# Kernel tuning notes

Hardware: AMD Instinct MI355X
Metric: run time of the kernel (lower is better)

Reference implementation:

```python
import jax, jax.numpy as jnp
import numpy as np

D_IN = 784
D_Z = 100
N_SAMP = 10
LOG_2PI = float(np.log(2.0 * np.pi))


def setup_inputs() -> dict:
    key = jax.random.key(0)
    ks = jax.random.split(key, 8)
    B = 16384
    x = jax.random.uniform(ks[0], (B, D_IN), dtype=jnp.float32)
    s = 0.05  # small init scale so softplus/sigmoid stay in a sane range
    W0 = jax.random.normal(ks[1], (D_Z, D_IN), dtype=jnp.float32) * s
    b0 = jax.random.normal(ks[2], (D_Z,), dtype=jnp.float32) * s
    W1 = jax.random.normal(ks[3], (D_Z, D_IN), dtype=jnp.float32) * s
    b1 = jax.random.normal(ks[4], (D_Z,), dtype=jnp.float32) * s
    W2 = jax.random.normal(ks[5], (D_IN, D_Z), dtype=jnp.float32) * s
    b2 = jax.random.normal(ks[6], (D_IN,), dtype=jnp.float32) * s
    eps = jax.random.normal(ks[7], (N_SAMP, D_Z), dtype=jnp.float32)  # pz.sample([10])
    return {"x": x, "W0": W0, "b0": b0, "W1": W1, "b1": b1, "W2": W2, "b2": b2, "eps": eps}


def reference(x, W0, b0, W1, b1, W2, b2, eps):
    # encoder: per-dim mean over the batch of softplus(Linear(x))
    mean = jnp.mean(jax.nn.softplus(x @ W0.T + b0), axis=0)        # [D_Z]
    cov = jnp.mean(jax.nn.softplus(x @ W1.T + b1), axis=0)         # [D_Z] (diag variances)
    # z = mean + covariance * eps, eps ~ N(0, I)
    z = mean + cov * eps                                           # [N_SAMP, D_Z]
    y = z @ W2.T + b2                                              # [N_SAMP, D_IN]
    p = jax.nn.sigmoid((2.0 * x[:, None, :] - 1.0) * y[None, :, :])  # [B, N_SAMP, D_IN]
    pv_z = jnp.prod(p, axis=-1) + 0.001                            # [B, N_SAMP]
    E_px_v = jnp.mean(jnp.log(pv_z))
    # diagonal-Gaussian log probs (equivalent to the MVN with eye*cov)
    log_pz = -0.5 * jnp.sum(z * z, axis=-1) - 0.5 * D_Z * LOG_2PI
    log_q = (-0.5 * jnp.sum((z - mean) ** 2 / cov, axis=-1)
             - 0.5 * jnp.sum(jnp.log(cov)) - 0.5 * D_Z * LOG_2PI)
    Dkl = jnp.mean(log_pz - log_q)
    return -(E_px_v + Dkl)
```

## Files before the change

kernel.cpp:

```cpp
#include <hip/hip_runtime.h>
#include <hip/hip_bf16.h>
#include <math.h>

#define NROWS 16384
#define DIN   784
#define DZ    100
#define NS    10
#define NCT   16
#define KTILES 25
#define BND_THR 45.0f

typedef unsigned short ushort_t;
typedef short bf16x8 __attribute__((ext_vector_type(8)));
typedef float f32x4  __attribute__((ext_vector_type(4)));

#define WS_Y2 208
#define WS_Z  8064
#define WB_OFF_BYTES (64u * 1024u)

__device__ __forceinline__ float softplus_fast(float v) {
    float t = v * 1.44269504088896f;
    return (fmaxf(t, 0.f)
            + __builtin_amdgcn_logf(1.f + __builtin_amdgcn_exp2f(-fabsf(t))))
           * 0.69314718055995f;
}
__device__ __forceinline__ unsigned pack2(float lo, float hi) {
    float2 f2; f2.x = lo; f2.y = hi;
    __hip_bfloat162 h2 = __float22bfloat162_rn(f2);
    return *reinterpret_cast<unsigned*>(&h2);
}

__global__ __launch_bounds__(256) void wb_kernel(
    const float* __restrict__ W0, const float* __restrict__ W1, ushort_t* __restrict__ Wb)
{
    int t = blockIdx.x * 256 + threadIdx.x;
    if (t >= KTILES * NCT * 64) return;
    int kt = t >> 10;
    int r  = t & 1023;
    int ct = r >> 6, l = r & 63;
    int col = ct * 16 + (l & 15);
    int k0  = kt * 32 + (l >> 4) * 8;
    uint4 o = make_uint4(0u, 0u, 0u, 0u);
    if (col < 200 && k0 < DIN) {
        const float* src = (col < 100 ? W0 + (size_t)col * DIN
                                      : W1 + (size_t)(col - 100) * DIN) + k0;
        float4 a = *(const float4*)src;
        float4 b = *(const float4*)(src + 4);
        o.x = pack2(a.x, a.y); o.y = pack2(a.z, a.w);
        o.z = pack2(b.x, b.y); o.w = pack2(b.z, b.w);
    }
    *(uint4*)(Wb + (size_t)t * 8) = o;
}

__global__ __launch_bounds__(512) void colmean_f(
    const float* __restrict__ x, const ushort_t* __restrict__ Wb,
    const float* __restrict__ b0, const float* __restrict__ b1,
    float* __restrict__ ws)
{
    __shared__ ushort_t xls[2 * KTILES * 512];
    const int tid = threadIdx.x;
    const int lane = tid & 63, w = tid >> 6;
    const int row0 = blockIdx.x * 32;

    for (int slot = tid; slot < 3200; slot += 512) {
        int r  = slot / 100;
        int sl = slot - r * 100;
        int kt = sl >> 2, kc = sl & 3;
        int k0 = kt * 32 + kc * 8;
        uint4 o = make_uint4(0u, 0u, 0u, 0u);
        if (k0 + 8 <= DIN) {
            const float* src = x + (size_t)(row0 + r) * DIN + k0;
            float4 a = *(const float4*)src, b = *(const float4*)(src + 4);
            o.x = pack2(a.x, a.y); o.y = pack2(a.z, a.w);
            o.z = pack2(b.x, b.y); o.w = pack2(b.z, b.w);
        }
        int l = (kc << 4) | (r & 15);
        *(uint4*)&xls[((size_t)(r >> 4) * KTILES + kt) * 512 + l * 8] = o;
    }
    __syncthreads();

    const int ct0 = w * 2;
    const ushort_t* a0p = xls + lane * 8;
    const ushort_t* a1p = xls + KTILES * 512 + lane * 8;
    const ushort_t* wbp = Wb + (size_t)ct0 * 512 + lane * 8;

    f32x4 acc00 = (f32x4){0.f,0.f,0.f,0.f}, acc01 = acc00;
    f32x4 acc10 = acc00, acc11 = acc00;

    bf16x8 A0a, A1a, A0b, A1b;
    uint4  B0a, B1a, B0b, B1b;

    auto ld = [&](int kt, bf16x8& A0, bf16x8& A1, uint4& B0, uint4& B1) {
        A0 = *(const bf16x8*)(a0p + (size_t)kt * 512);
        A1 = *(const bf16x8*)(a1p + (size_t)kt * 512);
        B0 = *(const uint4*)(wbp + (size_t)kt * 8192);
        B1 = *(const uint4*)(wbp + (size_t)kt * 8192 + 512);
    };
    auto cp = [&](const bf16x8& A0, const bf16x8& A1, const uint4& B0, const uint4& B1) {
        bf16x8 f0 = *(const bf16x8*)&B0, f1 = *(const bf16x8*)&B1;
        acc00 = __builtin_amdgcn_mfma_f32_16x16x32_bf16(A0, f0, acc00, 0, 0, 0);
        acc01 = __builtin_amdgcn_mfma_f32_16x16x32_bf16(A0, f1, acc01, 0, 0, 0);
        acc10 = __builtin_amdgcn_mfma_f32_16x16x32_bf16(A1, f0, acc10, 0, 0, 0);
        acc11 = __builtin_amdgcn_mfma_f32_16x16x32_bf16(A1, f1, acc11, 0, 0, 0);
    };

    ld(0, A0a, A1a, B0a, B1a);
    for (int i = 0; i < 12; ++i) {
        ld(2 * i + 1, A0b, A1b, B0b, B1b);
        cp(A0a, A1a, B0a, B1a);
        ld(2 * i + 2, A0a, A1a, B0a, B1a);
        cp(A0b, A1b, B0b, B1b);
    }
    cp(A0a, A1a, B0a, B1a);

    const int jcol = lane & 15;
#pragma unroll
    for (int ctl = 0; ctl < 2; ++ctl) {
        int j = (ct0 + ctl) * 16 + jcol;
        float bias = (j < 100) ? b0[j] : ((j < 200) ? b1[j - 100] : 0.f);
        f32x4 u0 = ctl ? acc01 : acc00;
        f32x4 u1 = ctl ? acc11 : acc10;
        float v = 0.f;
#pragma unroll
        for (int r = 0; r < 4; ++r)
            v += softplus_fast(u0[r] + bias) + softplus_fast(u1[r] + bias);
        v += __shfl_xor(v, 16);
        v += __shfl_xor(v, 32);
        if ((lane >> 4) == 0 && j < 200) atomicAdd(&ws[j], v);
    }
}

__global__ __launch_bounds__(256) void middle_kernel(
    const float* __restrict__ eps, float* __restrict__ ws)
{
    __shared__ float red[256];
    const int tid = threadIdx.x;
    float contrib = 0.f;
    if (tid < DZ) {
        const float inv = 1.f / (float)NROWS;
        float mm = ws[tid] * inv;
        float cc = ws[100 + tid] * inv;
        contrib = 0.5f * __logf(cc);
#pragma unroll
        for (int s = 0; s < NS; ++s) {
            float e = eps[s * DZ + tid];
            float zz = mm + cc * e;
            ws[WS_Z + s * DZ + tid] = zz;
            contrib += (0.5f * cc * e * e - 0.5f * zz * zz) * (1.f / NS);
        }
    }
    red[tid] = contrib;
    __syncthreads();
    for (int off = 128; off > 0; off >>= 1) {
        if (tid < off) red[tid] += red[tid + off];
        __syncthreads();
    }
    if (tid == 0) ws[201] = red[0];
}

__global__ __launch_bounds__(256) void y2_kernel(
    const float* __restrict__ W2, const float* __restrict__ b2,
    float* __restrict__ ws)
{
    int wid  = (int)((blockIdx.x * 256 + threadIdx.x) >> 6);
    int lane = threadIdx.x & 63;
    if (wid >= NS * DIN) return;
    int s = wid / DIN, i = wid % DIN;
    const float* zz = ws + WS_Z + s * DZ;
    const float* wr = W2 + (size_t)i * DZ;
    float p = 0.f;
    for (int d = lane; d < DZ; d += 64) p += zz[d] * wr[d];
#pragma unroll
    for (int off = 32; off > 0; off >>= 1) p += __shfl_xor(p, off);
    if (lane == 0) ws[WS_Y2 + wid] = (p + b2[i]) * 1.4426950408889634f;
}

__global__ __launch_bounds__(256, 4) void pv_kernel(
    const float* __restrict__ x, const float* ws, float* out_sum)
{
    __shared__ ushort_t yf[KTILES * 512];
    __shared__ ushort_t ya[KTILES * 512];
    __shared__ float bsum;
    const int tid = threadIdx.x;
    const int lane = tid & 63, w = tid >> 6;

    for (int idx = tid; idx < KTILES * 64; idx += 256) {
        int kt = idx >> 6, l = idx & 63;
        int ss = l & 15, k0 = kt * 32 + (l >> 4) * 8;
        uint4 o = make_uint4(0u, 0u, 0u, 0u), oa = o;
        if (ss < NS && k0 < DIN) {
            const float* src = ws + WS_Y2 + ss * DIN + k0;
            float4 a = *(const float4*)src, b = *(const float4*)(src + 4);
            o.x = pack2(a.x, a.y); o.y = pack2(a.z, a.w);
            o.z = pack2(b.x, b.y); o.w = pack2(b.z, b.w);
            oa.x = o.x & 0x7FFF7FFFu; oa.y = o.y & 0x7FFF7FFFu;
            oa.z = o.z & 0x7FFF7FFFu; oa.w = o.w & 0x7FFF7FFFu;
        }
        *(uint4*)(yf + (size_t)idx * 8) = o;
        *(uint4*)(ya + (size_t)idx * 8) = oa;
    }
    if (tid == 0) bsum = 0.f;
    __syncthreads();

    const int tile = blockIdx.x * 4 + w;
    const int row  = tile * 16 + (lane & 15);
    const int kc   = lane >> 4;
    const int s    = lane & 15;
    const float* xp = x + (size_t)row * DIN;
    const float L001 = -6.90775527898f;

    f32x4 acc0 = (f32x4){0.f, 0.f, 0.f, 0.f};
    f32x4 acc1 = (f32x4){0.f, 0.f, 0.f, 0.f};
    float4 a0A, a1A, a0B, a1B;

    auto loadA = [&](int kt, float4& a0, float4& a1) {
        int k0 = kt * 32 + kc * 8;
        if (k0 + 8 > DIN) k0 = 768;
        a0 = *(const float4*)(xp + k0);
        a1 = *(const float4*)(xp + k0 + 4);
    };
    auto comp = [&](int kt, const float4& a0, const float4& a1) {
        bf16x8 nf; unsigned* p = (unsigned*)&nf;
        p[0] = pack2(1.f - 2.f * a0.x, 1.f - 2.f * a0.y);
        p[1] = pack2(1.f - 2.f * a0.z, 1.f - 2.f * a0.w);
        p[2] = pack2(1.f - 2.f * a1.x, 1.f - 2.f * a1.y);
        p[3] = pack2(1.f - 2.f * a1.z, 1.f - 2.f * a1.w);
        bf16x8 na; unsigned* q = (unsigned*)&na;
        q[0] = p[0] & 0x7FFF7FFFu; q[1] = p[1] & 0x7FFF7FFFu;
        q[2] = p[2] & 0x7FFF7FFFu; q[3] = p[3] & 0x7FFF7FFFu;
        bf16x8 fy = *(const bf16x8*)(yf + (size_t)kt * 512 + lane * 8);
        bf16x8 fa = *(const bf16x8*)(ya + (size_t)kt * 512 + lane * 8);
        acc0 = __builtin_amdgcn_mfma_f32_16x16x32_bf16(nf, fy, acc0, 0, 0, 0);
        acc1 = __builtin_amdgcn_mfma_f32_16x16x32_bf16(na, fa, acc1, 0, 0, 0);
    };

    loadA(0, a0A, a1A);
    for (int i = 0; i < 12; ++i) {
        loadA(2 * i + 1, a0B, a1B);
        comp(2 * i, a0A, a1A);
        loadA(2 * i + 2, a0A, a1A);
        comp(2 * i + 1, a0B, a1B);
    }
    comp(24, a0A, a1A);

    float bnd[4];
#pragma unroll
    for (int r = 0; r < 4; ++r) bnd[r] = 0.5f * (acc0[r] + acc1[r]);

    float wsum;
    bool lslow = (s < NS) &&
        (fminf(fminf(bnd[0], bnd[1]), fminf(bnd[2], bnd[3])) < BND_THR);
    unsigned long long m = __ballot(lslow);
    if (m == 0ull) {
        wsum = 160.f * L001;
    } else {
        int nslow = 0;
        float slowsum = 0.f;
#pragma unroll
        for (int r = 0; r < 4; ++r) {
            unsigned long long mr = __ballot((s < NS) && (bnd[r] < BND_THR));
            nslow += (int)__popcll(mr);
            while (mr) {
                int src = (int)__ffsll(mr) - 1; mr &= (mr - 1);
                int ss = src & 15;
                int rrow = tile * 16 + (src >> 4) * 4 + r;
                const float* xq = x + (size_t)rrow * DIN;
                const float* yq = ws + WS_Y2 + ss * DIN;
                float a = 0.f;
                for (int i = lane; i < DIN; i += 64)
                    a -= __builtin_amdgcn_logf(
                        1.f + __builtin_amdgcn_exp2f((1.f - 2.f * xq[i]) * yq[i]));
#pragma unroll
                for (int off = 32; off > 0; off >>= 1) a += __shfl_xor(a, off);
                slowsum += __logf(__builtin_amdgcn_exp2f(a) + 0.001f);
            }
        }
        wsum = (float)(160 - nslow) * L001 + slowsum;
    }
    if (lane == 0) atomicAdd(&bsum, wsum);
    __syncthreads();
    if (tid == 0) atomicAdd(out_sum, bsum);
}

__global__ void final_kernel(const float* __restrict__ ws, float* __restrict__ out)
{
    float E = ws[200] * (1.f / ((float)NROWS * (float)NS));
    out[0] = -(E + ws[201]);
}

extern "C" void kernel_launch(void* const* d_in, const int* in_sizes, int n_in,
                              void* d_out, int out_size, void* d_ws, size_t ws_size,
                              hipStream_t stream)
{
    const float* x   = (const float*)d_in[0];
    const float* W0  = (const float*)d_in[1];
    const float* b0  = (const float*)d_in[2];
    const float* W1  = (const float*)d_in[3];
    const float* b1  = (const float*)d_in[4];
    const float* W2  = (const float*)d_in[5];
    const float* b2  = (const float*)d_in[6];
    const float* eps = (const float*)d_in[7];
    float* out = (float*)d_out;
    float* ws  = (float*)d_ws;
    ushort_t* Wb = (ushort_t*)((char*)d_ws + WB_OFF_BYTES);

    hipMemsetAsync(ws, 0, 512 * sizeof(float), stream);
    wb_kernel<<<(KTILES * NCT * 64 + 255) / 256, 256, 0, stream>>>(W0, W1, Wb);
    colmean_f<<<NROWS / 32, 512, 0, stream>>>(x, Wb, b0, b1, ws);
    middle_kernel<<<1, 256, 0, stream>>>(eps, ws);
    y2_kernel<<<(NS * DIN * 64) / 256, 256, 0, stream>>>(W2, b2, ws);
    pv_kernel<<<256, 256, 0, stream>>>(x, ws, ws + 200);
    final_kernel<<<1, 1, 0, stream>>>(ws, out);
}
```

Measured before the change: 61.41 us.

## Fuse small kernels: fold memset, middle and final stages into neighbors

Removes the memset, middle_kernel and final_kernel launches. Zeroing of the workspace moves into wb_kernel block 0, and z is computed inline inside the y2 kernel. The KL term and final output are computed by the last-finishing pv block, found with an atomic counter and threadfence. This cuts launch count and serialization gaps between tiny kernels, at the cost of redundant z computation per warp and a last-block pattern that relies on correct memory ordering.

```diff
diff --git a/kernel.cpp b/kernel.cpp
--- a/kernel.cpp
+++ b/kernel.cpp
@@ -15,7 +15,6 @@
 typedef float f32x4  __attribute__((ext_vector_type(4)));
 
 #define WS_Y2 208
-#define WS_Z  8064
 #define WB_OFF_BYTES (64u * 1024u)
 
 __device__ __forceinline__ float softplus_fast(float v) {
@@ -31,8 +30,10 @@
 }
 
 __global__ __launch_bounds__(256) void wb_kernel(
-    const float* __restrict__ W0, const float* __restrict__ W1, ushort_t* __restrict__ Wb)
-{
+    const float* __restrict__ W0, const float* __restrict__ W1,
+    ushort_t* __restrict__ Wb, float* __restrict__ ws)
+{
+    if (blockIdx.x == 0) ws[threadIdx.x] = 0.f;
     int t = blockIdx.x * 256 + threadIdx.x;
     if (t >= KTILES * NCT * 64) return;
     int kt = t >> 10;
@@ -130,57 +131,36 @@
     }
 }
 
-__global__ __launch_bounds__(256) void middle_kernel(
+__global__ __launch_bounds__(256) void y2z_kernel(
+    const float* __restrict__ W2, const float* __restrict__ b2,
     const float* __restrict__ eps, float* __restrict__ ws)
-{
-    __shared__ float red[256];
-    const int tid = threadIdx.x;
-    float contrib = 0.f;
-    if (tid < DZ) {
-        const float inv = 1.f / (float)NROWS;
-        float mm = ws[tid] * inv;
-        float cc = ws[100 + tid] * inv;
-        contrib = 0.5f * __logf(cc);
-#pragma unroll
-        for (int s = 0; s < NS; ++s) {
-            float e = eps[s * DZ + tid];
-            float zz = mm + cc * e;
-            ws[WS_Z + s * DZ + tid] = zz;
-            contrib += (0.5f * cc * e * e - 0.5f * zz * zz) * (1.f / NS);
-        }
-    }
-    red[tid] = contrib;
-    __syncthreads();
-    for (int off = 128; off > 0; off >>= 1) {
-        if (tid < off) red[tid] += red[tid + off];
-        __syncthreads();
-    }
-    if (tid == 0) ws[201] = red[0];
-}
-
-__global__ __launch_bounds__(256) void y2_kernel(
-    const float* __restrict__ W2, const float* __restrict__ b2,
-    float* __restrict__ ws)
 {
     int wid  = (int)((blockIdx.x * 256 + threadIdx.x) >> 6);
     int lane = threadIdx.x & 63;
     if (wid >= NS * DIN) return;
     int s = wid / DIN, i = wid % DIN;
-    const float* zz = ws + WS_Z + s * DZ;
+    const float inv = 1.f / (float)NROWS;
     const float* wr = W2 + (size_t)i * DZ;
+    const float* er = eps + (size_t)s * DZ;
     float p = 0.f;
-    for (int d = lane; d < DZ; d += 64) p += zz[d] * wr[d];
+    for (int d = lane; d < DZ; d += 64) {
+        float zd = inv * (ws[d] + ws[100 + d] * er[d]);
+        p += zd * wr[d];
+    }
 #pragma unroll
     for (int off = 32; off > 0; off >>= 1) p += __shfl_xor(p, off);
     if (lane == 0) ws[WS_Y2 + wid] = (p + b2[i]) * 1.4426950408889634f;
 }
 
-__global__ __launch_bounds__(256, 4) void pv_kernel(
-    const float* __restrict__ x, const float* ws, float* out_sum)
+__global__ __launch_bounds__(256, 4) void pv_final_kernel(
+    const float* __restrict__ x, float* __restrict__ ws,
+    const float* __restrict__ eps, float* __restrict__ out, int nblocks)
 {
     __shared__ ushort_t yf[KTILES * 512];
     __shared__ ushort_t ya[KTILES * 512];
     __shared__ float bsum;
+    __shared__ int lastflag;
+    __shared__ float dred[256];
     const int tid = threadIdx.x;
     const int lane = tid & 63, w = tid >> 6;
 
@@ -199,7 +179,7 @@
         *(uint4*)(yf + (size_t)idx * 8) = o;
         *(uint4*)(ya + (size_t)idx * 8) = oa;
     }
-    if (tid == 0) bsum = 0.f;
+    if (tid == 0) { bsum = 0.f; lastflag = 0; }
     __syncthreads();
 
     const int tile = blockIdx.x * 4 + w;
@@ -279,13 +259,41 @@
     }
     if (lane == 0) atomicAdd(&bsum, wsum);
     __syncthreads();
-    if (tid == 0) atomicAdd(out_sum, bsum);
-}
-
-__global__ void final_kernel(const float* __restrict__ ws, float* __restrict__ out)
-{
-    float E = ws[200] * (1.f / ((float)NROWS * (float)NS));
-    out[0] = -(E + ws[201]);
+
+    if (tid == 0) {
+        atomicAdd(&ws[200], bsum);
+        __threadfence();
+        unsigned old = atomicAdd((unsigned*)&ws[202], 1u);
+        if (old == (unsigned)(nblocks - 1)) lastflag = 1;
+    }
+    __syncthreads();
+    if (lastflag) {
+        __threadfence();
+        float contrib = 0.f;
+        if (tid < DZ) {
+            const float inv = 1.f / (float)NROWS;
+            float mm = ws[tid] * inv;
+            float cc = ws[100 + tid] * inv;
+            contrib = 0.5f * __logf(cc);
+#pragma unroll
+            for (int ss2 = 0; ss2 < NS; ++ss2) {
+                float e = eps[ss2 * DZ + tid];
+                float zz = mm + cc * e;
+                contrib += (0.5f * cc * e * e - 0.5f * zz * zz) * (1.f / NS);
+            }
+        }
+        dred[tid] = contrib;
+        __syncthreads();
+        for (int off = 128; off > 0; off >>= 1) {
+            if (tid < off) dred[tid] += dred[tid + off];
+            __syncthreads();
+        }
+        if (tid == 0) {
+            float S = atomicAdd(&ws[200], 0.f);
+            float E = S * (1.f / ((float)NROWS * (float)NS));
+            out[0] = -(E + dred[0]);
+        }
+    }
 }
 
 extern "C" void kernel_launch(void* const* d_in, const int* in_sizes, int n_in,
@@ -304,11 +312,8 @@
     float* ws  = (float*)d_ws;
     ushort_t* Wb = (ushort_t*)((char*)d_ws + WB_OFF_BYTES);
 
-    hipMemsetAsync(ws, 0, 512 * sizeof(float), stream);
-    wb_kernel<<<(KTILES * NCT * 64 + 255) / 256, 256, 0, stream>>>(W0, W1, Wb);
+    wb_kernel<<<(KTILES * NCT * 64 + 255) / 256, 256, 0, stream>>>(W0, W1, Wb, ws);
     colmean_f<<<NROWS / 32, 512, 0, stream>>>(x, Wb, b0, b1, ws);
-    middle_kernel<<<1, 256, 0, stream>>>(eps, ws);
-    y2_kernel<<<(NS * DIN * 64) / 256, 256, 0, stream>>>(W2, b2, ws);
-    pv_kernel<<<256, 256, 0, stream>>>(x, ws, ws + 200);
-    final_kernel<<<1, 1, 0, stream>>>(ws, out);
-}
+    y2z_kernel<<<(NS * DIN * 64) / 256, 256, 0, stream>>>(W2, b2, eps, ws);
+    pv_final_kernel<<<256, 256, 0, stream>>>(x, ws, eps, out, 256);
+}
```

Measured after the change: 60.13 us. -2.1%, faster.
